# Kernel tuning notes

Measured on AMD Instinct MI355X. Metric: run time of the kernel, lower is better.

## Reference

```python
import jax, jax.numpy as jnp
import numpy as np

D_IN = 256
DIMS = 256


def setup_inputs() -> dict:
    key = jax.random.key(0)
    k1, k2, k3, k4, k5 = jax.random.split(key, 5)
    B, Tq, Tk = 4, 512, 512
    query = jax.random.normal(k1, (B, Tq, D_IN), dtype=jnp.float32)
    value = jax.random.normal(k2, (B, Tk, D_IN), dtype=jnp.float32)
    # Dense(dims, use_bias=False) kernels (glorot-like scale) and AdditiveAttention scale vector
    Wq = jax.random.normal(k3, (D_IN, DIMS), dtype=jnp.float32) / np.sqrt(D_IN)
    Wv = jax.random.normal(k4, (D_IN, DIMS), dtype=jnp.float32) / np.sqrt(D_IN)
    scale = jax.random.normal(k5, (DIMS,), dtype=jnp.float32)
    return {"query": query, "value": value, "Wq": Wq, "Wv": Wv, "scale": scale}


def reference(query, value, Wq, Wv, scale):
    # q_proj: [B,Tq,d], k_proj: [B,Tk,d]; attention value = RAW value tensor (as in source)
    q = jnp.einsum("bqi,id->bqd", query, Wq)
    k = jnp.einsum("bki,id->bkd", value, Wv)
    # Additive (Bahdanau) scores: [B,Tq,Tk] via broadcast tanh then reduce with scale
    scores = jnp.einsum("bqkd,d->bqk", jnp.tanh(q[:, :, None, :] + k[:, None, :, :]), scale)
    attn = jax.nn.softmax(scores, axis=-1)  # masks are all-ones -> no-op
    out = jnp.einsum("bqk,bki->bqi", attn, value)
    return out, attn
```

## Files before the change

kernel.cpp:

```cpp
#include <hip/hip_runtime.h>

#define LOG2E 1.4426950408889634f
#define TWO_LOG2E 2.885390081777927f

__device__ __forceinline__ float fast_exp2(float x) { return __builtin_amdgcn_exp2f(x); }
__device__ __forceinline__ float fast_rcp(float x)  { return __builtin_amdgcn_rcpf(x); }

__global__ __launch_bounds__(256) void proj_kernel(
    const float* __restrict__ query, const float* __restrict__ value,
    const float* __restrict__ Wq, const float* __restrict__ Wv,
    float* __restrict__ eq, float* __restrict__ ek)
{
    __shared__ float in_lds[8 * 256];
    const int t = threadIdx.x;
    const int row0 = blockIdx.x * 8;
    const float* src; const float* W; float* dst;
    if (row0 < 2048) { src = query + (size_t)row0 * 256; W = Wq; dst = eq + (size_t)row0 * 256; }
    else { const int r = row0 - 2048; src = value + (size_t)r * 256; W = Wv; dst = ek + (size_t)r * 256; }

    const float4* s4 = (const float4*)src;
    float4* l4 = (float4*)in_lds;
    l4[t] = s4[t];
    l4[t + 256] = s4[t + 256];
    __syncthreads();

    float acc[8];
#pragma unroll
    for (int r = 0; r < 8; ++r) acc[r] = 0.f;

    for (int d = 0; d < 256; d += 4) {
        const float w0 = W[(d + 0) * 256 + t];
        const float w1 = W[(d + 1) * 256 + t];
        const float w2 = W[(d + 2) * 256 + t];
        const float w3 = W[(d + 3) * 256 + t];
#pragma unroll
        for (int r = 0; r < 8; ++r) {
            const float4 v = *(const float4*)&in_lds[r * 256 + d];
            acc[r] = fmaf(v.x, w0, acc[r]);
            acc[r] = fmaf(v.y, w1, acc[r]);
            acc[r] = fmaf(v.z, w2, acc[r]);
            acc[r] = fmaf(v.w, w3, acc[r]);
        }
    }
#pragma unroll
    for (int r = 0; r < 8; ++r) dst[r * 256 + t] = fast_exp2(acc[r] * TWO_LOG2E);
}

#define SQ_ST 130
__global__ __launch_bounds__(256) void scores_kernel(
    const float* __restrict__ eq, const float* __restrict__ ek,
    const float* __restrict__ scale,
    float* __restrict__ part0, float* __restrict__ part1)
{
    __shared__ float q_lds[32 * SQ_ST];
    __shared__ float k_lds[32 * SQ_ST];
    __shared__ float sc_lds[128];

    const int t = threadIdx.x;
    const int tx = t & 15, ty = t >> 4;
    const int kt = blockIdx.x, qt = blockIdx.y;
    const int b = blockIdx.z >> 1, dh = blockIdx.z & 1;
    const int d0 = dh * 128;
    const float* qbase = eq + (size_t)(b * 512 + qt * 32) * 256 + d0;
    const float* kbase = ek + (size_t)(b * 512 + kt * 32) * 256 + d0;

    if (t < 128) sc_lds[t] = -2.f * scale[d0 + t];

#pragma unroll
    for (int l = 0; l < 4; ++l) {
        const int idx = t + 256 * l;
        const int row = idx >> 5, c4 = (idx & 31) * 4;
        const float4 qv = *(const float4*)&qbase[row * 256 + c4];
        const float4 kv = *(const float4*)&kbase[row * 256 + c4];
        *(float2*)&q_lds[row * SQ_ST + c4]     = make_float2(qv.x, qv.y);
        *(float2*)&q_lds[row * SQ_ST + c4 + 2] = make_float2(qv.z, qv.w);
        *(float2*)&k_lds[row * SQ_ST + c4]     = make_float2(kv.x, kv.y);
        *(float2*)&k_lds[row * SQ_ST + c4 + 2] = make_float2(kv.z, kv.w);
    }
    __syncthreads();

    float a00 = 0.f, a01 = 0.f, a10 = 0.f, a11 = 0.f;

#pragma unroll 4
    for (int d = 0; d < 128; d += 2) {
        const float2 s2 = *(const float2*)&sc_lds[d];
        const float2 qa = *(const float2*)&q_lds[(ty * 2 + 0) * SQ_ST + d];
        const float2 qb = *(const float2*)&q_lds[(ty * 2 + 1) * SQ_ST + d];
        const float2 ka = *(const float2*)&k_lds[(tx * 2 + 0) * SQ_ST + d];
        const float2 kb = *(const float2*)&k_lds[(tx * 2 + 1) * SQ_ST + d];

        {
            const float A = fmaf(qa.x, ka.x, 1.f), B = fmaf(qa.y, ka.y, 1.f);
            a00 = fmaf(fmaf(s2.y, A, s2.x * B), fast_rcp(A * B), a00);
        }
        {
            const float A = fmaf(qa.x, kb.x, 1.f), B = fmaf(qa.y, kb.y, 1.f);
            a01 = fmaf(fmaf(s2.y, A, s2.x * B), fast_rcp(A * B), a01);
        }
        {
            const float A = fmaf(qb.x, ka.x, 1.f), B = fmaf(qb.y, ka.y, 1.f);
            a10 = fmaf(fmaf(s2.y, A, s2.x * B), fast_rcp(A * B), a10);
        }
        {
            const float A = fmaf(qb.x, kb.x, 1.f), B = fmaf(qb.y, kb.y, 1.f);
            a11 = fmaf(fmaf(s2.y, A, s2.x * B), fast_rcp(A * B), a11);
        }
    }

    float* part = dh ? part1 : part0;
    const int qrow = qt * 32 + ty * 2;
    const int kcol = kt * 32 + tx * 2;
    *(float2*)&part[(size_t)(b * 512 + qrow + 0) * 512 + kcol] = make_float2(a00, a01);
    *(float2*)&part[(size_t)(b * 512 + qrow + 1) * 512 + kcol] = make_float2(a10, a11);
}

#define ST_ROW 516
__global__ __launch_bounds__(512) void softpv_kernel(
    const float* __restrict__ part0, const float* __restrict__ part1,
    const float* __restrict__ value,
    float* __restrict__ attn, float* __restrict__ out)
{
    __shared__ float s_tile[8 * ST_ROW];
    __shared__ float v_lds[64 * 256];
    __shared__ float inv_lds[8];

    const int t = threadIdx.x;
    const int qt = blockIdx.x, b = blockIdx.y;
    const int q0 = qt * 8;
    const size_t rowbase = (size_t)(b * 512 + q0) * 512;

    {
        const float4* p0 = (const float4*)(part0 + rowbase);
        const float4* p1 = (const float4*)(part1 + rowbase);
#pragma unroll
        for (int l = 0; l < 2; ++l) {
            const int idx = t + 512 * l;
            const int row = idx >> 7, c4 = idx & 127;
            float4 a = p0[idx];
            const float4 c = p1[idx];
            a.x += c.x; a.y += c.y; a.z += c.z; a.w += c.w;
            *(float4*)&s_tile[row * ST_ROW + c4 * 4] = a;
        }
    }
    __syncthreads();

    const int w = t >> 6, lane = t & 63;
    {
        float e[8];
        float m = -1e30f;
#pragma unroll
        for (int j = 0; j < 8; ++j) {
            e[j] = s_tile[w * ST_ROW + lane + 64 * j];
            m = fmaxf(m, e[j]);
        }
#pragma unroll
        for (int off = 32; off; off >>= 1) m = fmaxf(m, __shfl_xor(m, off));

        float sum = 0.f;
#pragma unroll
        for (int j = 0; j < 8; ++j) {
            e[j] = fast_exp2((e[j] - m) * LOG2E);
            sum += e[j];
        }
#pragma unroll
        for (int off = 32; off; off >>= 1) sum += __shfl_xor(sum, off);

        const float inv = fast_rcp(sum);
        float* arow = attn + rowbase + (size_t)w * 512;
#pragma unroll
        for (int j = 0; j < 8; ++j) {
            s_tile[w * ST_ROW + lane + 64 * j] = e[j];
            arow[lane + 64 * j] = e[j] * inv;
        }
        if (lane == 0) inv_lds[w] = inv;
    }

    const int r = lane >> 3;
    const int c = 32 * w + (lane & 7) * 4;
    float4 acc = {0.f, 0.f, 0.f, 0.f};

    for (int kc = 0; kc < 512; kc += 64) {
        __syncthreads();
        const float4* vsrc = (const float4*)(value + (size_t)(b * 512 + kc) * 256);
#pragma unroll
        for (int l = 0; l < 8; ++l) {
            const int idx = t + 512 * l;
            *(float4*)&v_lds[idx * 4] = vsrc[idx];
        }
        __syncthreads();

#pragma unroll 4
        for (int k = 0; k < 64; ++k) {
            const float s = s_tile[r * ST_ROW + kc + k];
            const float4 v = *(const float4*)&v_lds[k * 256 + c];
            acc.x = fmaf(s, v.x, acc.x);
            acc.y = fmaf(s, v.y, acc.y);
            acc.z = fmaf(s, v.z, acc.z);
            acc.w = fmaf(s, v.w, acc.w);
        }
    }

    const float inv = inv_lds[r];
    acc.x *= inv; acc.y *= inv; acc.z *= inv; acc.w *= inv;
    *(float4*)&out[(size_t)(b * 512 + q0 + r) * 256 + c] = acc;
}

extern "C" void kernel_launch(void* const* d_in, const int* in_sizes, int n_in,
                              void* d_out, int out_size, void* d_ws, size_t ws_size,
                              hipStream_t stream) {
    const float* query = (const float*)d_in[0];
    const float* value = (const float*)d_in[1];
    const float* Wq    = (const float*)d_in[2];
    const float* Wv    = (const float*)d_in[3];
    const float* scale = (const float*)d_in[4];

    float* out0 = (float*)d_out;
    float* attn = out0 + 4 * 512 * 256;

    float* eq    = (float*)d_ws;
    float* ek    = eq + 2048 * 256;
    float* part0 = ek + 2048 * 256;
    float* part1 = part0 + 4 * 512 * 512;

    proj_kernel<<<512, 256, 0, stream>>>(query, value, Wq, Wv, eq, ek);
    scores_kernel<<<dim3(16, 16, 8), 256, 0, stream>>>(eq, ek, scale, part0, part1);
    softpv_kernel<<<dim3(64, 4), 512, 0, stream>>>(part0, part1, value, attn, out0);
}
```

Before: 75.56 us.

## Drop split-D partial score buffers; write raw scores into attn and split-K PV

```diff
diff --git a/kernel.cpp b/kernel.cpp
--- a/kernel.cpp
+++ b/kernel.cpp
@@ -47,162 +47,193 @@
 }
 
 #define SQ_ST 130
-__global__ __launch_bounds__(256) void scores_kernel(
+__global__ __launch_bounds__(512) void scores_kernel(
     const float* __restrict__ eq, const float* __restrict__ ek,
-    const float* __restrict__ scale,
-    float* __restrict__ part0, float* __restrict__ part1)
+    const float* __restrict__ scale, float* __restrict__ sraw)
 {
     __shared__ float q_lds[32 * SQ_ST];
-    __shared__ float k_lds[32 * SQ_ST];
-    __shared__ float sc_lds[128];
+    __shared__ float k_lds[64 * SQ_ST];
+    __shared__ float sc_lds[256];
 
     const int t = threadIdx.x;
-    const int tx = t & 15, ty = t >> 4;
-    const int kt = blockIdx.x, qt = blockIdx.y;
-    const int b = blockIdx.z >> 1, dh = blockIdx.z & 1;
-    const int d0 = dh * 128;
-    const float* qbase = eq + (size_t)(b * 512 + qt * 32) * 256 + d0;
-    const float* kbase = ek + (size_t)(b * 512 + kt * 32) * 256 + d0;
-
-    if (t < 128) sc_lds[t] = -2.f * scale[d0 + t];
-
-#pragma unroll
-    for (int l = 0; l < 4; ++l) {
-        const int idx = t + 256 * l;
-        const int row = idx >> 5, c4 = (idx & 31) * 4;
-        const float4 qv = *(const float4*)&qbase[row * 256 + c4];
-        const float4 kv = *(const float4*)&kbase[row * 256 + c4];
-        *(float2*)&q_lds[row * SQ_ST + c4]     = make_float2(qv.x, qv.y);
-        *(float2*)&q_lds[row * SQ_ST + c4 + 2] = make_float2(qv.z, qv.w);
-        *(float2*)&k_lds[row * SQ_ST + c4]     = make_float2(kv.x, kv.y);
-        *(float2*)&k_lds[row * SQ_ST + c4 + 2] = make_float2(kv.z, kv.w);
-    }
-    __syncthreads();
+    const int tx = t & 31, ty = t >> 5;
+    const int ktg = blockIdx.x, qt = blockIdx.y, b = blockIdx.z;
+    const float* qbase = eq + (size_t)(b * 512 + qt * 32) * 256;
+    const float* kbase = ek + (size_t)(b * 512 + ktg * 64) * 256;
+
+    if (t < 256) sc_lds[t] = -2.f * scale[t];
 
     float a00 = 0.f, a01 = 0.f, a10 = 0.f, a11 = 0.f;
 
+    for (int dc = 0; dc < 256; dc += 128) {
+        __syncthreads();
+#pragma unroll
+        for (int l = 0; l < 2; ++l) {
+            const int idx = t + 512 * l;
+            const int row = idx >> 5, c4 = (idx & 31) * 4;
+            const float4 v = *(const float4*)&qbase[row * 256 + dc + c4];
+            *(float2*)&q_lds[row * SQ_ST + c4]     = make_float2(v.x, v.y);
+            *(float2*)&q_lds[row * SQ_ST + c4 + 2] = make_float2(v.z, v.w);
+        }
+#pragma unroll
+        for (int l = 0; l < 4; ++l) {
+            const int idx = t + 512 * l;
+            const int row = idx >> 5, c4 = (idx & 31) * 4;
+            const float4 v = *(const float4*)&kbase[row * 256 + dc + c4];
+            *(float2*)&k_lds[row * SQ_ST + c4]     = make_float2(v.x, v.y);
+            *(float2*)&k_lds[row * SQ_ST + c4 + 2] = make_float2(v.z, v.w);
+        }
+        __syncthreads();
+
 #pragma unroll 4
-    for (int d = 0; d < 128; d += 2) {
-        const float2 s2 = *(const float2*)&sc_lds[d];
-        const float2 qa = *(const float2*)&q_lds[(ty * 2 + 0) * SQ_ST + d];
-        const float2 qb = *(const float2*)&q_lds[(ty * 2 + 1) * SQ_ST + d];
-        const float2 ka = *(const float2*)&k_lds[(tx * 2 + 0) * SQ_ST + d];
-        const float2 kb = *(const float2*)&k_lds[(tx * 2 + 1) * SQ_ST + d];
-
-        {
-            const float A = fmaf(qa.x, ka.x, 1.f), B = fmaf(qa.y, ka.y, 1.f);
-            a00 = fmaf(fmaf(s2.y, A, s2.x * B), fast_rcp(A * B), a00);
-        }
-        {
-            const float A = fmaf(qa.x, kb.x, 1.f), B = fmaf(qa.y, kb.y, 1.f);
-            a01 = fmaf(fmaf(s2.y, A, s2.x * B), fast_rcp(A * B), a01);
-        }
-        {
-            const float A = fmaf(qb.x, ka.x, 1.f), B = fmaf(qb.y, ka.y, 1.f);
-            a10 = fmaf(fmaf(s2.y, A, s2.x * B), fast_rcp(A * B), a10);
-        }
-        {
-            const float A = fmaf(qb.x, kb.x, 1.f), B = fmaf(qb.y, kb.y, 1.f);
-            a11 = fmaf(fmaf(s2.y, A, s2.x * B), fast_rcp(A * B), a11);
-        }
-    }
-
-    float* part = dh ? part1 : part0;
-    const int qrow = qt * 32 + ty * 2;
-    const int kcol = kt * 32 + tx * 2;
-    *(float2*)&part[(size_t)(b * 512 + qrow + 0) * 512 + kcol] = make_float2(a00, a01);
-    *(float2*)&part[(size_t)(b * 512 + qrow + 1) * 512 + kcol] = make_float2(a10, a11);
-}
-
-#define ST_ROW 516
+        for (int d = 0; d < 128; d += 2) {
+            const float2 s2 = *(const float2*)&sc_lds[dc + d];
+            const float2 qa = *(const float2*)&q_lds[(ty * 2 + 0) * SQ_ST + d];
+            const float2 qb = *(const float2*)&q_lds[(ty * 2 + 1) * SQ_ST + d];
+            const float2 ka = *(const float2*)&k_lds[tx * SQ_ST + d];
+            const float2 kb = *(const float2*)&k_lds[(tx + 32) * SQ_ST + d];
+
+            {
+                const float A = fmaf(qa.x, ka.x, 1.f), B = fmaf(qa.y, ka.y, 1.f);
+                a00 = fmaf(fmaf(s2.y, A, s2.x * B), fast_rcp(A * B), a00);
+            }
+            {
+                const float A = fmaf(qa.x, kb.x, 1.f), B = fmaf(qa.y, kb.y, 1.f);
+                a01 = fmaf(fmaf(s2.y, A, s2.x * B), fast_rcp(A * B), a01);
+            }
+            {
+                const float A = fmaf(qb.x, ka.x, 1.f), B = fmaf(qb.y, ka.y, 1.f);
+                a10 = fmaf(fmaf(s2.y, A, s2.x * B), fast_rcp(A * B), a10);
+            }
+            {
+                const float A = fmaf(qb.x, kb.x, 1.f), B = fmaf(qb.y, kb.y, 1.f);
+                a11 = fmaf(fmaf(s2.y, A, s2.x * B), fast_rcp(A * B), a11);
+            }
+        }
+    }
+
+    const int qrow = b * 512 + qt * 32 + ty * 2;
+    const int kcol = ktg * 64 + tx;
+    sraw[(size_t)(qrow + 0) * 512 + kcol]      = a00;
+    sraw[(size_t)(qrow + 0) * 512 + kcol + 32] = a01;
+    sraw[(size_t)(qrow + 1) * 512 + kcol]      = a10;
+    sraw[(size_t)(qrow + 1) * 512 + kcol + 32] = a11;
+}
+
+#define SS_ROW 516
 __global__ __launch_bounds__(512) void softpv_kernel(
-    const float* __restrict__ part0, const float* __restrict__ part1,
-    const float* __restrict__ value,
-    float* __restrict__ attn, float* __restrict__ out)
+    float* __restrict__ attn, const float* __restrict__ value,
+    float* __restrict__ out)
 {
-    __shared__ float s_tile[8 * ST_ROW];
-    __shared__ float v_lds[64 * 256];
+    __shared__ float s_lds[8 * SS_ROW];
+    __shared__ float red[4 * 8 * 256];
     __shared__ float inv_lds[8];
 
     const int t = threadIdx.x;
+    const int w = t >> 6, lane = t & 63;
     const int qt = blockIdx.x, b = blockIdx.y;
     const int q0 = qt * 8;
-    const size_t rowbase = (size_t)(b * 512 + q0) * 512;
-
-    {
-        const float4* p0 = (const float4*)(part0 + rowbase);
-        const float4* p1 = (const float4*)(part1 + rowbase);
-#pragma unroll
-        for (int l = 0; l < 2; ++l) {
-            const int idx = t + 512 * l;
-            const int row = idx >> 7, c4 = idx & 127;
-            float4 a = p0[idx];
-            const float4 c = p1[idx];
-            a.x += c.x; a.y += c.y; a.z += c.z; a.w += c.w;
-            *(float4*)&s_tile[row * ST_ROW + c4 * 4] = a;
-        }
-    }
-    __syncthreads();
-
-    const int w = t >> 6, lane = t & 63;
-    {
-        float e[8];
-        float m = -1e30f;
-#pragma unroll
-        for (int j = 0; j < 8; ++j) {
-            e[j] = s_tile[w * ST_ROW + lane + 64 * j];
-            m = fmaxf(m, e[j]);
-        }
-#pragma unroll
-        for (int off = 32; off; off >>= 1) m = fmaxf(m, __shfl_xor(m, off));
-
-        float sum = 0.f;
-#pragma unroll
-        for (int j = 0; j < 8; ++j) {
-            e[j] = fast_exp2((e[j] - m) * LOG2E);
-            sum += e[j];
-        }
-#pragma unroll
-        for (int off = 32; off; off >>= 1) sum += __shfl_xor(sum, off);
-
-        const float inv = fast_rcp(sum);
-        float* arow = attn + rowbase + (size_t)w * 512;
-#pragma unroll
-        for (int j = 0; j < 8; ++j) {
-            s_tile[w * ST_ROW + lane + 64 * j] = e[j];
-            arow[lane + 64 * j] = e[j] * inv;
-        }
-        if (lane == 0) inv_lds[w] = inv;
-    }
-
-    const int r = lane >> 3;
-    const int c = 32 * w + (lane & 7) * 4;
-    float4 acc = {0.f, 0.f, 0.f, 0.f};
-
-    for (int kc = 0; kc < 512; kc += 64) {
-        __syncthreads();
-        const float4* vsrc = (const float4*)(value + (size_t)(b * 512 + kc) * 256);
-#pragma unroll
-        for (int l = 0; l < 8; ++l) {
-            const int idx = t + 512 * l;
-            *(float4*)&v_lds[idx * 4] = vsrc[idx];
-        }
-        __syncthreads();
-
-#pragma unroll 4
-        for (int k = 0; k < 64; ++k) {
-            const float s = s_tile[r * ST_ROW + kc + k];
-            const float4 v = *(const float4*)&v_lds[k * 256 + c];
-            acc.x = fmaf(s, v.x, acc.x);
-            acc.y = fmaf(s, v.y, acc.y);
-            acc.z = fmaf(s, v.z, acc.z);
-            acc.w = fmaf(s, v.w, acc.w);
-        }
-    }
-
-    const float inv = inv_lds[r];
-    acc.x *= inv; acc.y *= inv; acc.z *= inv; acc.w *= inv;
-    *(float4*)&out[(size_t)(b * 512 + q0 + r) * 256 + c] = acc;
+    float* srow = attn + (size_t)(b * 512 + q0 + w) * 512;
+
+    float e[8];
+    float m = -1e30f;
+#pragma unroll
+    for (int j = 0; j < 8; ++j) {
+        e[j] = srow[lane + 64 * j];
+        m = fmaxf(m, e[j]);
+    }
+#pragma unroll
+    for (int off = 32; off; off >>= 1) m = fmaxf(m, __shfl_xor(m, off));
+
+    float sum = 0.f;
+#pragma unroll
+    for (int j = 0; j < 8; ++j) {
+        e[j] = fast_exp2((e[j] - m) * LOG2E);
+        sum += e[j];
+    }
+#pragma unroll
+    for (int off = 32; off; off >>= 1) sum += __shfl_xor(sum, off);
+
+    const float inv = fast_rcp(sum);
+#pragma unroll
+    for (int j = 0; j < 8; ++j) {
+        s_lds[w * SS_ROW + lane + 64 * j] = e[j];
+        srow[lane + 64 * j] = e[j] * inv;
+    }
+    if (lane == 0) inv_lds[w] = inv;
+    __syncthreads();
+
+    float4 acc[8];
+#pragma unroll
+    for (int r = 0; r < 8; ++r) acc[r] = make_float4(0.f, 0.f, 0.f, 0.f);
+
+    const float* vbase = value + (size_t)(b * 512 + 64 * w) * 256;
+    for (int k4 = 0; k4 < 64; k4 += 4) {
+        const float4 v0 = *(const float4*)&vbase[(k4 + 0) * 256 + lane * 4];
+        const float4 v1 = *(const float4*)&vbase[(k4 + 1) * 256 + lane * 4];
+        const float4 v2 = *(const float4*)&vbase[(k4 + 2) * 256 + lane * 4];
+        const float4 v3 = *(const float4*)&vbase[(k4 + 3) * 256 + lane * 4];
+#pragma unroll
+        for (int r = 0; r < 8; ++r) {
+            const float4 s4 = *(const float4*)&s_lds[r * SS_ROW + 64 * w + k4];
+            acc[r].x = fmaf(s4.x, v0.x, acc[r].x); acc[r].y = fmaf(s4.x, v0.y, acc[r].y);
+            acc[r].z = fmaf(s4.x, v0.z, acc[r].z); acc[r].w = fmaf(s4.x, v0.w, acc[r].w);
+            acc[r].x = fmaf(s4.y, v1.x, acc[r].x); acc[r].y = fmaf(s4.y, v1.y, acc[r].y);
+            acc[r].z = fmaf(s4.y, v1.z, acc[r].z); acc[r].w = fmaf(s4.y, v1.w, acc[r].w);
+            acc[r].x = fmaf(s4.z, v2.x, acc[r].x); acc[r].y = fmaf(s4.z, v2.y, acc[r].y);
+            acc[r].z = fmaf(s4.z, v2.z, acc[r].z); acc[r].w = fmaf(s4.z, v2.w, acc[r].w);
+            acc[r].x = fmaf(s4.w, v3.x, acc[r].x); acc[r].y = fmaf(s4.w, v3.y, acc[r].y);
+            acc[r].z = fmaf(s4.w, v3.z, acc[r].z); acc[r].w = fmaf(s4.w, v3.w, acc[r].w);
+        }
+    }
+
+    if (w >= 4) {
+#pragma unroll
+        for (int r = 0; r < 8; ++r)
+            *(float4*)&red[((w - 4) * 8 + r) * 256 + lane * 4] = acc[r];
+    }
+    __syncthreads();
+    if (w < 4) {
+#pragma unroll
+        for (int r = 0; r < 8; ++r) {
+            const float4 o = *(const float4*)&red[(w * 8 + r) * 256 + lane * 4];
+            acc[r].x += o.x; acc[r].y += o.y; acc[r].z += o.z; acc[r].w += o.w;
+        }
+    }
+    __syncthreads();
+    if (w >= 2 && w < 4) {
+#pragma unroll
+        for (int r = 0; r < 8; ++r)
+            *(float4*)&red[((w - 2) * 8 + r) * 256 + lane * 4] = acc[r];
+    }
+    __syncthreads();
+    if (w < 2) {
+#pragma unroll
+        for (int r = 0; r < 8; ++r) {
+            const float4 o = *(const float4*)&red[(w * 8 + r) * 256 + lane * 4];
+            acc[r].x += o.x; acc[r].y += o.y; acc[r].z += o.z; acc[r].w += o.w;
+        }
+    }
+    __syncthreads();
+    if (w == 1) {
+#pragma unroll
+        for (int r = 0; r < 8; ++r)
+            *(float4*)&red[r * 256 + lane * 4] = acc[r];
+    }
+    __syncthreads();
+    if (w == 0) {
+#pragma unroll
+        for (int r = 0; r < 8; ++r) {
+            const float4 o = *(const float4*)&red[r * 256 + lane * 4];
+            const float iv = inv_lds[r];
+            float4 res;
+            res.x = (acc[r].x + o.x) * iv;
+            res.y = (acc[r].y + o.y) * iv;
+            res.z = (acc[r].z + o.z) * iv;
+            res.w = (acc[r].w + o.w) * iv;
+            *(float4*)&out[(size_t)(b * 512 + q0 + r) * 256 + lane * 4] = res;
+        }
+    }
 }
 
 extern "C" void kernel_launch(void* const* d_in, const int* in_sizes, int n_in,
@@ -217,12 +248,10 @@
     float* out0 = (float*)d_out;
     float* attn = out0 + 4 * 512 * 256;
 
-    float* eq    = (float*)d_ws;
-    float* ek    = eq + 2048 * 256;
-    float* part0 = ek + 2048 * 256;
-    float* part1 = part0 + 4 * 512 * 512;
+    float* eq = (float*)d_ws;
+    float* ek = eq + 2048 * 256;
 
     proj_kernel<<<512, 256, 0, stream>>>(query, value, Wq, Wv, eq, ek);
-    scores_kernel<<<dim3(16, 16, 8), 256, 0, stream>>>(eq, ek, scale, part0, part1);
-    softpv_kernel<<<dim3(64, 4), 512, 0, stream>>>(part0, part1, value, attn, out0);
-}
+    scores_kernel<<<dim3(8, 16, 4), 512, 0, stream>>>(eq, ek, scale, attn);
+    softpv_kernel<<<dim3(64, 4), 512, 0, stream>>>(attn, value, out0);
+}
```

New measurement: 69.76 us. -7.7%, faster.
